# Kernel optimization log

Hardware: AMD Instinct MI355X
Metric: run time of the kernel (lower is better)

The kernel has to match this reference:

```python
import jax, jax.numpy as jnp
import numpy as np

N = 3072
FEAT = 128
E = 24576


def setup_inputs() -> dict:
    key = jax.random.key(0)
    k1, k2, k3, k4 = jax.random.split(key, 4)
    x = jax.random.normal(k1, (N, FEAT), dtype=jnp.float32)
    edge_index = jax.random.randint(k2, (2, E), 0, N, dtype=jnp.int32)
    batch = jnp.zeros((N,), dtype=jnp.int32)
    # lin: Linear(2*FEAT, 1)
    w = jax.random.normal(k3, (2 * FEAT,), dtype=jnp.float32) / np.sqrt(2 * FEAT)
    b = jax.random.normal(k4, (), dtype=jnp.float32) * 0.01
    return {"x": x, "edge_index": edge_index, "batch": batch, "w": w, "b": b}


def _cc_labels(adj):
    """Connected-component labels via min-label propagation + pointer jumping.
    Labels equal the minimum node index of each component, so ranking them by
    value reproduces scipy's first-occurrence component ordering."""
    n = adj.shape[0]
    adj = jax.lax.stop_gradient(adj)

    def body(state):
        labels, _ = state
        neigh = jnp.where(adj > 0, labels[None, :], n).min(axis=1)  # [n]
        new = jnp.minimum(labels, neigh)
        new = jnp.minimum(new, new[new])  # pointer jumping
        return new, jnp.any(new != labels)

    labels, _ = jax.lax.while_loop(lambda s: s[1], body,
                                   (jnp.arange(n), jnp.array(True)))
    return labels


def reference(x, edge_index, batch, w, b):
    n, f = x.shape
    idx = jnp.arange(n)
    src, dst = edge_index[0], edge_index[1]
    # undirected: duplicate each edge in both directions (coalesce in the
    # original dedups; dense scatter-set below is equivalent since duplicate
    # (u,v) edges get identical scores)
    s2 = jnp.concatenate([src, dst])
    d2 = jnp.concatenate([dst, src])
    # per-edge raw score: lin(concat(x[u], x[v]))  ->  tanh
    e = jnp.tanh(x[s2] @ w[:f] + x[d2] @ w[f:] + b)  # [2E]

    zero = jnp.zeros((n, n), dtype=x.dtype)
    A = zero.at[s2, d2].set(1.0).at[idx, idx].set(0.0)   # self-loops removed
    S = zero.at[s2, d2].set(e).at[idx, idx].set(0.0)
    contract = (e > 0.0).astype(x.dtype)                 # tanh -> threshold 0
    A_c = zero.at[s2, d2].max(contract).at[idx, idx].set(0.0)

    labels = _cc_labels(A_c)                             # min-node-index labels
    roots = (labels == idx).astype(jnp.int32)
    cluster = (jnp.cumsum(roots) - 1)[labels]            # consecutive 0..K-1
    C = jax.nn.one_hot(cluster, n, dtype=x.dtype)        # [n, n] (padded to n)

    single = (A_c.sum(axis=1) + A_c.sum(axis=0)) == 0    # isolated under contraction
    S = S.at[idx, idx].set(single.astype(x.dtype))

    X_new = (S @ C).T @ x                                # [n(padK), f]
    A_new = (C.T @ A @ C).at[idx, idx].set(0.0)          # dense coarsened adjacency
    new_batch = jnp.zeros((n,), dtype=batch.dtype).at[cluster].max(batch)
    return X_new, A_new, new_batch, cluster
```

## Files before the change

### kernel.cpp

```cpp
#include <hip/hip_runtime.h>
#include <math.h>

#define N 3072
#define FEAT 128
#define NE 24576
#define PSTRIDE 64
#define EPT 24
#define DOTB 768
#define OUTZ4 2458368
#define ZB3 608
#define GATB 192

__device__ __forceinline__ void wave_agg_add(bool valid, int key, float val,
                                             float* base, int stride, int off) {
    int lane = threadIdx.x & 63;
    unsigned long long active = __ballot(valid ? 1 : 0);
    while (active) {
        int leader = __ffsll(active) - 1;
        int lkey = __shfl(key, leader);
        bool mine = valid && (key == lkey);
        unsigned long long grp = __ballot(mine ? 1 : 0);
        float v = mine ? val : 0.0f;
        #pragma unroll
        for (int o = 32; o; o >>= 1) v += __shfl_xor(v, o);
        if (lane == leader)
            atomicAdd(&base[(size_t)lkey * stride + off], v);
        active &= ~grp;
    }
}

__global__ void k_init(const float* __restrict__ x, const float* __restrict__ w,
                       float* __restrict__ a, float* __restrict__ c,
                       float4* __restrict__ zws) {
    int b = blockIdx.x, t = threadIdx.x;
    if (b < DOTB) {
        int node = b * 4 + (t >> 6);
        int lane = t & 63;
        const float* xi = x + node * FEAT;
        float pa = xi[lane] * w[lane] + xi[lane + 64] * w[lane + 64];
        float pc = xi[lane] * w[FEAT + lane] + xi[lane + 64] * w[FEAT + lane + 64];
        for (int off = 32; off; off >>= 1) {
            pa += __shfl_down(pa, off);
            pc += __shfl_down(pc, off);
        }
        if (lane == 0) { a[node] = pa; c[node] = pc; }
    } else {
        float4 z = {0.f, 0.f, 0.f, 0.f};
        #pragma unroll
        for (int k = 0; k < 6; ++k) zws[k * 256 + t] = z;
    }
}

__global__ void k_edge_pairs(const int* __restrict__ ei, const float* __restrict__ a,
                             const float* __restrict__ c, const float* __restrict__ bb,
                             unsigned* __restrict__ ep, int* __restrict__ notsingle,
                             int* __restrict__ pcnt, unsigned long long* __restrict__ ptab) {
    int t = blockIdx.x * blockDim.x + threadIdx.x;
    if (t >= NE) return;
    int u = ei[t], v = ei[NE + t];
    unsigned wpk = (unsigned)u | ((unsigned)v << 12);
    if (u != v) {
        float b = bb[0];
        float su = a[u] + c[v] + b;
        float sv = a[v] + c[u] + b;
        unsigned fu = (su > 0.f) ? 1u : 0u;
        unsigned fv = (sv > 0.f) ? 1u : 0u;
        wpk |= (fu << 24) | (fv << 25);
        if (fu | fv) { notsingle[u] = 1; notsingle[v] = 1; }
        float eu = tanhf(su);
        int sl = atomicAdd(&pcnt[v], 1);
        if (sl < PSTRIDE)
            ptab[(size_t)v * PSTRIDE + sl] =
                ((unsigned long long)__float_as_uint(eu) << 32) | (unsigned)u;
        float ev2 = tanhf(sv);
        sl = atomicAdd(&pcnt[u], 1);
        if (sl < PSTRIDE)
            ptab[(size_t)u * PSTRIDE + sl] =
                ((unsigned long long)__float_as_uint(ev2) << 32) | (unsigned)v;
    }
    ep[t] = wpk;
}

__global__ void __launch_bounds__(1024)
k_prop_gather(const unsigned* __restrict__ ep, const float* __restrict__ x,
              const int* __restrict__ pcnt, const unsigned long long* __restrict__ ptab,
              const int* __restrict__ notsingle, float* __restrict__ y,
              unsigned long long* __restrict__ qmask, int* __restrict__ cluster,
              float* __restrict__ out_cluster, float4* __restrict__ zout) {
    __shared__ int lab[N];
    __shared__ int ssum[1024];
    __shared__ unsigned short rk[N];
    __shared__ int sh_p[16 * 64];
    __shared__ int flag;
    int t = threadIdx.x, blk = blockIdx.x;
    int wv = t >> 6, lane = t & 63;
    if (blk == 0) {
        unsigned er[EPT];
        unsigned act = 0;
        #pragma unroll
        for (int j = 0; j < EPT; ++j) {
            er[j] = ep[t + j * 1024];
            if (er[j] & 0x3000000u) act |= (1u << j);
        }
        for (int i = t; i < N; i += 1024) lab[i] = i;
        for (;;) {
            __syncthreads();
            if (t == 0) flag = 0;
            __syncthreads();
            unsigned rem = act;
            while (rem) {
                int j = __ffs(rem) - 1;
                rem &= rem - 1;
                unsigned wpk = er[j];
                int u = wpk & 0xFFF, v = (wpk >> 12) & 0xFFF;
                int lu = lab[u], lv = lab[v];
                if ((lu | lv) == 0) { act &= ~(1u << j); continue; }
                if ((wpk & (1u << 24)) && lv < lu) { atomicMin(&lab[u], lv); flag = 1; }
                if ((wpk & (1u << 25)) && lu < lv) { atomicMin(&lab[v], lu); flag = 1; }
            }
            for (int i = t; i < N; i += 1024) {
                int m = lab[i];
                if (m == 0) continue;
                int mm = lab[m];
                while (mm < m) { m = mm; mm = lab[m]; }
                if (m < lab[i]) { atomicMin(&lab[i], m); flag = 1; }
            }
            __syncthreads();
            if (!flag) break;
        }
        int i0 = 3 * t;
        int r0 = (lab[i0] == i0);
        int r1 = (lab[i0 + 1] == i0 + 1);
        int r2 = (lab[i0 + 2] == i0 + 2);
        int s = r0 + r1 + r2;
        ssum[t] = s;
        __syncthreads();
        for (int off = 1; off < 1024; off <<= 1) {
            int val = (t >= off) ? ssum[t - off] : 0;
            __syncthreads();
            ssum[t] += val;
            __syncthreads();
        }
        int run = ssum[t] - s;
        run += r0; rk[i0]     = (unsigned short)(run - 1);
        run += r1; rk[i0 + 1] = (unsigned short)(run - 1);
        run += r2; rk[i0 + 2] = (unsigned short)(run - 1);
        __syncthreads();
        for (int j = t; j < N; j += 1024) {
            int cl = rk[lab[j]];
            cluster[j] = cl;
            out_cluster[j] = (float)cl;
        }
    } else if (blk <= GATB) {
        int q = (blk - 1) * 16 + wv;
        int cnt = pcnt[q]; if (cnt > PSTRIDE) cnt = PSTRIDE;
        const unsigned long long* row = ptab + (size_t)q * PSTRIDE;
        int myp = -1 - lane;
        float mye = 0.f;
        if (lane < cnt) {
            unsigned long long s = row[lane];
            myp = (int)(s & 0xFFFFFFFFu);
            mye = __uint_as_float((unsigned)(s >> 32));
        }
        sh_p[wv * 64 + lane] = myp;
        bool dup = false;
        for (int j = 0; j < lane && !dup; ++j)
            dup = (sh_p[wv * 64 + j] == myp);
        bool valid = (lane < cnt) && !dup;
        unsigned long long m = __ballot(valid ? 1 : 0);
        if (lane == 0) qmask[q] = m;
        float acc0 = 0.f, acc1 = 0.f;
        for (int j = 0; j < cnt; ++j) {
            if (!((m >> j) & 1ull)) continue;
            int p = __shfl(myp, j);
            float e = __shfl(mye, j);
            const float* xp = x + p * FEAT;
            acc0 += e * xp[lane];
            acc1 += e * xp[lane + 64];
        }
        if (!notsingle[q]) {
            const float* xq = x + q * FEAT;
            acc0 += xq[lane];
            acc1 += xq[lane + 64];
        }
        float* yq = y + q * FEAT;
        yq[lane] = acc0;
        yq[lane + 64] = acc1;
    } else {
        float4 z = {0.f, 0.f, 0.f, 0.f};
        int base = (blk - GATB - 1) * 4096;
        #pragma unroll
        for (int k = 0; k < 4; ++k) {
            int idx = base + k * 1024 + t;
            if (idx < OUTZ4) zout[idx] = z;
        }
    }
}

__global__ void k_reduce_anew(const float* __restrict__ y, const int* __restrict__ cluster,
                              const int* __restrict__ pcnt,
                              const unsigned long long* __restrict__ ptab,
                              const unsigned long long* __restrict__ qmask,
                              float* __restrict__ Xnew, float* __restrict__ Anew) {
    int gid = blockIdx.x * blockDim.x + threadIdx.x;
    int wid = gid >> 6, lane = gid & 63;
    if (wid < 6144) {
        int f = wid & (FEAT - 1);
        int chunk = wid >> 7;
        int q = chunk * 64 + lane;
        wave_agg_add(true, cluster[q], y[q * FEAT + f], Xnew, FEAT, f);
    } else {
        int q = wid - 6144;
        int cnt = pcnt[q]; if (cnt > PSTRIDE) cnt = PSTRIDE;
        unsigned long long m = qmask[q];
        bool valid = (lane < cnt) && ((m >> lane) & 1ull);
        int p = 0;
        if (valid) p = (int)(ptab[(size_t)q * PSTRIDE + lane] & 0xFFFFFFFFu);
        int cq = cluster[q];
        int cp = valid ? cluster[p] : 0;
        valid = valid && (cp != cq);
        wave_agg_add(valid, cp * N + cq, 1.0f, Anew, 1, 0);
    }
}

extern "C" void kernel_launch(void* const* d_in, const int* in_sizes, int n_in,
                              void* d_out, int out_size, void* d_ws, size_t ws_size,
                              hipStream_t stream) {
    const float* x  = (const float*)d_in[0];
    const int*   ei = (const int*)d_in[1];
    const float* w  = (const float*)d_in[3];
    const float* bb = (const float*)d_in[4];

    char* ws = (char*)d_ws;
    size_t off = 0;
    int* pcnt     = (int*)(ws + off);      off += (size_t)N * 4;
    int* notsing  = (int*)(ws + off);      off += (size_t)N * 4;
    float* a      = (float*)(ws + off);    off += (size_t)N * 4;
    float* c      = (float*)(ws + off);    off += (size_t)N * 4;
    int* cluster  = (int*)(ws + off);      off += (size_t)N * 4;
    unsigned* ep  = (unsigned*)(ws + off); off += (size_t)NE * 4;
    unsigned long long* qmask = (unsigned long long*)(ws + off); off += (size_t)N * 8;
    float* y      = (float*)(ws + off);    off += (size_t)N * FEAT * 4;
    unsigned long long* ptab = (unsigned long long*)(ws + off); off += (size_t)N * PSTRIDE * 8;

    float* Xnew        = (float*)d_out;
    float* Anew        = Xnew + (size_t)N * FEAT;
    float* out_cluster = Anew + (size_t)N * N + N;

    k_init<<<DOTB + 1, 256, 0, stream>>>(x, w, a, c, (float4*)ws);
    k_edge_pairs<<<NE / 256, 256, 0, stream>>>(ei, a, c, bb, ep, notsing, pcnt, ptab);
    k_prop_gather<<<1 + GATB + ZB3, 1024, 0, stream>>>(ep, x, pcnt, ptab, notsing, y,
                                                       qmask, cluster, out_cluster,
                                                       (float4*)d_out);
    k_reduce_anew<<<(9216 * 64) / 1024, 1024, 0, stream>>>(y, cluster, pcnt, ptab,
                                                           qmask, Xnew, Anew);
}
```

Before: 146.2 us.

## Fuse four kernels into two using grid-level spin-wait flags

Merges the dot-product, edge-pair and output-zeroing kernels into one launch, where the edge blocks spin on an atomic counter until every dot block has finished. It also merges label propagation, neighbor gather and the Xnew/Anew atomic reduction into one launch, where all blocks wait on completion counters before the reduction phase. The edge-relaxation loop is unrolled into forward and reverse sweeps over register-held edges, which may cut the number of propagation rounds. The aim is to remove launch and inter-kernel gaps. In exchange the reduction now runs on far fewer waves, and the spin-waits assume all blocks are co-resident, which risks a hang if they are not.

Result: slower. 284.6 us (+94.6%).

```diff
diff --git a/kernel.cpp b/kernel.cpp
--- a/kernel.cpp
+++ b/kernel.cpp
@@ -5,11 +5,16 @@
 #define FEAT 128
 #define NE 24576
 #define PSTRIDE 64
-#define EPT 24
 #define DOTB 768
+#define EDGB 96
 #define OUTZ4 2458368
-#define ZB3 608
+#define OZB 2401
 #define GATB 192
+#define K2B (1 + GATB)
+#define RWAVES (K2B * 16)
+
+#define FOR24(M)  M(0)M(1)M(2)M(3)M(4)M(5)M(6)M(7)M(8)M(9)M(10)M(11)M(12)M(13)M(14)M(15)M(16)M(17)M(18)M(19)M(20)M(21)M(22)M(23)
+#define FOR24R(M) M(23)M(22)M(21)M(20)M(19)M(18)M(17)M(16)M(15)M(14)M(13)M(12)M(11)M(10)M(9)M(8)M(7)M(6)M(5)M(4)M(3)M(2)M(1)M(0)
 
 __device__ __forceinline__ void wave_agg_add(bool valid, int key, float val,
                                              float* base, int stride, int off) {
@@ -29,11 +34,21 @@
     }
 }
 
-__global__ void k_init(const float* __restrict__ x, const float* __restrict__ w,
-                       float* __restrict__ a, float* __restrict__ c,
-                       float4* __restrict__ zws) {
+__device__ __forceinline__ int ctrl_ld(const int* p) {
+    return __hip_atomic_load(p, __ATOMIC_RELAXED, __HIP_MEMORY_SCOPE_AGENT);
+}
+
+__global__ void k_initez(const float* __restrict__ x, const float* __restrict__ w,
+                         const int* __restrict__ ei, const float* __restrict__ bb,
+                         float* __restrict__ a, float* __restrict__ c,
+                         unsigned* __restrict__ ep, int* __restrict__ notsingle,
+                         int* __restrict__ pcnt, unsigned long long* __restrict__ ptab,
+                         float4* __restrict__ zout, float4* __restrict__ zws,
+                         int* __restrict__ ctrl) {
     int b = blockIdx.x, t = threadIdx.x;
     if (b < DOTB) {
+        float4 z = {0.f, 0.f, 0.f, 0.f};
+        if (b < 6) zws[b * 256 + t] = z;
         int node = b * 4 + (t >> 6);
         int lane = t & 63;
         const float* xi = x + node * FEAT;
@@ -44,49 +59,55 @@
             pc += __shfl_down(pc, off);
         }
         if (lane == 0) { a[node] = pa; c[node] = pc; }
+        __syncthreads();
+        __threadfence();
+        if (t == 0) atomicAdd(&ctrl[0], 1);
+    } else if (b < DOTB + EDGB) {
+        if (t == 0)
+            while (ctrl_ld(&ctrl[0]) < DOTB) __builtin_amdgcn_s_sleep(2);
+        __syncthreads();
+        __threadfence();
+        int s = (b - DOTB) * 256 + t;
+        int u = ei[s], v = ei[NE + s];
+        unsigned wpk = (unsigned)u | ((unsigned)v << 12);
+        if (u != v) {
+            float bias = bb[0];
+            float su = a[u] + c[v] + bias;
+            float sv = a[v] + c[u] + bias;
+            unsigned fu = (su > 0.f) ? 1u : 0u;
+            unsigned fv = (sv > 0.f) ? 1u : 0u;
+            wpk |= (fu << 24) | (fv << 25);
+            if (fu | fv) { notsingle[u] = 1; notsingle[v] = 1; }
+            float eu = tanhf(su);
+            int sl = atomicAdd(&pcnt[v], 1);
+            if (sl < PSTRIDE)
+                ptab[(size_t)v * PSTRIDE + sl] =
+                    ((unsigned long long)__float_as_uint(eu) << 32) | (unsigned)u;
+            float ev2 = tanhf(sv);
+            sl = atomicAdd(&pcnt[u], 1);
+            if (sl < PSTRIDE)
+                ptab[(size_t)u * PSTRIDE + sl] =
+                    ((unsigned long long)__float_as_uint(ev2) << 32) | (unsigned)v;
+        }
+        ep[s] = wpk;
     } else {
         float4 z = {0.f, 0.f, 0.f, 0.f};
+        int base = (b - DOTB - EDGB) * 1024;
         #pragma unroll
-        for (int k = 0; k < 6; ++k) zws[k * 256 + t] = z;
-    }
-}
-
-__global__ void k_edge_pairs(const int* __restrict__ ei, const float* __restrict__ a,
-                             const float* __restrict__ c, const float* __restrict__ bb,
-                             unsigned* __restrict__ ep, int* __restrict__ notsingle,
-                             int* __restrict__ pcnt, unsigned long long* __restrict__ ptab) {
-    int t = blockIdx.x * blockDim.x + threadIdx.x;
-    if (t >= NE) return;
-    int u = ei[t], v = ei[NE + t];
-    unsigned wpk = (unsigned)u | ((unsigned)v << 12);
-    if (u != v) {
-        float b = bb[0];
-        float su = a[u] + c[v] + b;
-        float sv = a[v] + c[u] + b;
-        unsigned fu = (su > 0.f) ? 1u : 0u;
-        unsigned fv = (sv > 0.f) ? 1u : 0u;
-        wpk |= (fu << 24) | (fv << 25);
-        if (fu | fv) { notsingle[u] = 1; notsingle[v] = 1; }
-        float eu = tanhf(su);
-        int sl = atomicAdd(&pcnt[v], 1);
-        if (sl < PSTRIDE)
-            ptab[(size_t)v * PSTRIDE + sl] =
-                ((unsigned long long)__float_as_uint(eu) << 32) | (unsigned)u;
-        float ev2 = tanhf(sv);
-        sl = atomicAdd(&pcnt[u], 1);
-        if (sl < PSTRIDE)
-            ptab[(size_t)u * PSTRIDE + sl] =
-                ((unsigned long long)__float_as_uint(ev2) << 32) | (unsigned)v;
-    }
-    ep[t] = wpk;
+        for (int k = 0; k < 4; ++k) {
+            int idx = base + k * 256 + t;
+            if (idx < OUTZ4) zout[idx] = z;
+        }
+    }
 }
 
 __global__ void __launch_bounds__(1024)
-k_prop_gather(const unsigned* __restrict__ ep, const float* __restrict__ x,
-              const int* __restrict__ pcnt, const unsigned long long* __restrict__ ptab,
-              const int* __restrict__ notsingle, float* __restrict__ y,
-              unsigned long long* __restrict__ qmask, int* __restrict__ cluster,
-              float* __restrict__ out_cluster, float4* __restrict__ zout) {
+k_pgr(const unsigned* __restrict__ ep, const float* __restrict__ x,
+      const int* __restrict__ pcnt, const unsigned long long* __restrict__ ptab,
+      const int* __restrict__ notsingle, float* __restrict__ y,
+      unsigned long long* __restrict__ qmask, int* __restrict__ cluster,
+      float* __restrict__ out_cluster, float* __restrict__ Xnew,
+      float* __restrict__ Anew, int* __restrict__ ctrl) {
     __shared__ int lab[N];
     __shared__ int ssum[1024];
     __shared__ unsigned short rk[N];
@@ -95,29 +116,26 @@
     int t = threadIdx.x, blk = blockIdx.x;
     int wv = t >> 6, lane = t & 63;
     if (blk == 0) {
-        unsigned er[EPT];
         unsigned act = 0;
-        #pragma unroll
-        for (int j = 0; j < EPT; ++j) {
-            er[j] = ep[t + j * 1024];
-            if (er[j] & 0x3000000u) act |= (1u << j);
-        }
+        #define LDE(j) unsigned e##j = ep[t + (j) * 1024]; \
+                       if (e##j & 0x3000000u) act |= (1u << (j));
+        FOR24(LDE)
         for (int i = t; i < N; i += 1024) lab[i] = i;
         for (;;) {
             __syncthreads();
             if (t == 0) flag = 0;
             __syncthreads();
-            unsigned rem = act;
-            while (rem) {
-                int j = __ffs(rem) - 1;
-                rem &= rem - 1;
-                unsigned wpk = er[j];
-                int u = wpk & 0xFFF, v = (wpk >> 12) & 0xFFF;
-                int lu = lab[u], lv = lab[v];
-                if ((lu | lv) == 0) { act &= ~(1u << j); continue; }
-                if ((wpk & (1u << 24)) && lv < lu) { atomicMin(&lab[u], lv); flag = 1; }
-                if ((wpk & (1u << 25)) && lu < lv) { atomicMin(&lab[v], lu); flag = 1; }
-            }
+            #define RLX(j) if (act & (1u << (j))) { \
+                int u_ = (int)(e##j & 0xFFFu); \
+                int v_ = (int)((e##j >> 12) & 0xFFFu); \
+                int lu_ = lab[u_], lv_ = lab[v_]; \
+                if ((lu_ | lv_) == 0) { act &= ~(1u << (j)); } \
+                else { \
+                    if ((e##j & (1u << 24)) && lv_ < lu_) { atomicMin(&lab[u_], lv_); flag = 1; } \
+                    if ((e##j & (1u << 25)) && lu_ < lv_) { atomicMin(&lab[v_], lu_); flag = 1; } \
+                } }
+            FOR24(RLX)
+            FOR24R(RLX)
             for (int i = t; i < N; i += 1024) {
                 int m = lab[i];
                 if (m == 0) continue;
@@ -151,7 +169,10 @@
             cluster[j] = cl;
             out_cluster[j] = (float)cl;
         }
-    } else if (blk <= GATB) {
+        __syncthreads();
+        __threadfence();
+        if (t == 0) atomicAdd(&ctrl[2], 1);
+    } else {
         int q = (blk - 1) * 16 + wv;
         int cnt = pcnt[q]; if (cnt > PSTRIDE) cnt = PSTRIDE;
         const unsigned long long* row = ptab + (size_t)q * PSTRIDE;
@@ -186,40 +207,34 @@
         float* yq = y + q * FEAT;
         yq[lane] = acc0;
         yq[lane + 64] = acc1;
-    } else {
-        float4 z = {0.f, 0.f, 0.f, 0.f};
-        int base = (blk - GATB - 1) * 4096;
-        #pragma unroll
-        for (int k = 0; k < 4; ++k) {
-            int idx = base + k * 1024 + t;
-            if (idx < OUTZ4) zout[idx] = z;
-        }
-    }
-}
-
-__global__ void k_reduce_anew(const float* __restrict__ y, const int* __restrict__ cluster,
-                              const int* __restrict__ pcnt,
-                              const unsigned long long* __restrict__ ptab,
-                              const unsigned long long* __restrict__ qmask,
-                              float* __restrict__ Xnew, float* __restrict__ Anew) {
-    int gid = blockIdx.x * blockDim.x + threadIdx.x;
-    int wid = gid >> 6, lane = gid & 63;
-    if (wid < 6144) {
-        int f = wid & (FEAT - 1);
-        int chunk = wid >> 7;
-        int q = chunk * 64 + lane;
-        wave_agg_add(true, cluster[q], y[q * FEAT + f], Xnew, FEAT, f);
-    } else {
-        int q = wid - 6144;
-        int cnt = pcnt[q]; if (cnt > PSTRIDE) cnt = PSTRIDE;
-        unsigned long long m = qmask[q];
-        bool valid = (lane < cnt) && ((m >> lane) & 1ull);
-        int p = 0;
-        if (valid) p = (int)(ptab[(size_t)q * PSTRIDE + lane] & 0xFFFFFFFFu);
-        int cq = cluster[q];
-        int cp = valid ? cluster[p] : 0;
-        valid = valid && (cp != cq);
-        wave_agg_add(valid, cp * N + cq, 1.0f, Anew, 1, 0);
+        __syncthreads();
+        __threadfence();
+        if (t == 0) atomicAdd(&ctrl[1], 1);
+    }
+    if (t == 0) {
+        while (ctrl_ld(&ctrl[1]) < GATB) __builtin_amdgcn_s_sleep(2);
+        while (ctrl_ld(&ctrl[2]) < 1)    __builtin_amdgcn_s_sleep(2);
+    }
+    __syncthreads();
+    __threadfence();
+    for (int gw = blk * 16 + wv; gw < 9216; gw += RWAVES) {
+        if (gw < 6144) {
+            int f = gw & (FEAT - 1);
+            int chunk = gw >> 7;
+            int q = chunk * 64 + lane;
+            wave_agg_add(true, cluster[q], y[q * FEAT + f], Xnew, FEAT, f);
+        } else {
+            int q = gw - 6144;
+            int cnt = pcnt[q]; if (cnt > PSTRIDE) cnt = PSTRIDE;
+            unsigned long long m = qmask[q];
+            bool valid = (lane < cnt) && ((m >> lane) & 1ull);
+            int p = 0;
+            if (valid) p = (int)(ptab[(size_t)q * PSTRIDE + lane] & 0xFFFFFFFFu);
+            int cq = cluster[q];
+            int cp = valid ? cluster[p] : 0;
+            valid = valid && (cp != cq);
+            wave_agg_add(valid, cp * N + cq, 1.0f, Anew, 1, 0);
+        }
     }
 }
 
@@ -233,6 +248,7 @@
 
     char* ws = (char*)d_ws;
     size_t off = 0;
+    int* ctrl     = (int*)(ws + off);      off += 16;
     int* pcnt     = (int*)(ws + off);      off += (size_t)N * 4;
     int* notsing  = (int*)(ws + off);      off += (size_t)N * 4;
     float* a      = (float*)(ws + off);    off += (size_t)N * 4;
@@ -247,11 +263,10 @@
     float* Anew        = Xnew + (size_t)N * FEAT;
     float* out_cluster = Anew + (size_t)N * N + N;
 
-    k_init<<<DOTB + 1, 256, 0, stream>>>(x, w, a, c, (float4*)ws);
-    k_edge_pairs<<<NE / 256, 256, 0, stream>>>(ei, a, c, bb, ep, notsing, pcnt, ptab);
-    k_prop_gather<<<1 + GATB + ZB3, 1024, 0, stream>>>(ep, x, pcnt, ptab, notsing, y,
-                                                       qmask, cluster, out_cluster,
-                                                       (float4*)d_out);
-    k_reduce_anew<<<(9216 * 64) / 1024, 1024, 0, stream>>>(y, cluster, pcnt, ptab,
-                                                           qmask, Xnew, Anew);
-}
+    hipMemsetAsync(ctrl, 0, 16, stream);
+    k_initez<<<DOTB + EDGB + OZB, 256, 0, stream>>>(x, w, ei, bb, a, c, ep, notsing,
+                                                    pcnt, ptab, (float4*)d_out,
+                                                    (float4*)pcnt, ctrl);
+    k_pgr<<<K2B, 1024, 0, stream>>>(ep, x, pcnt, ptab, notsing, y, qmask, cluster,
+                                    out_cluster, Xnew, Anew, ctrl);
+}
```

## Split connected-component labeling into giant-component BFS plus residual label propagation

Applied to the files above, without the earlier changes.

The single-block component labeling now first grows the component containing node 0 as a shared-memory bitmask, using directed reachability over the contracted edges. It then collects the leftover edges and nodes outside that component into compact shared lists and runs min-label propagation with pointer jumping only over them, falling back to a full edge sweep if the residual list overflows. The aim is to cut the per-iteration cost of label propagation, since the giant component is settled cheaply with bit operations. In exchange, edges are reloaded from global memory instead of held in registers, and shared memory use and code complexity both grow.

New measurement: 134.0 us. 1.09x faster.

```diff
diff --git a/kernel.cpp b/kernel.cpp
--- a/kernel.cpp
+++ b/kernel.cpp
@@ -5,11 +5,11 @@
 #define FEAT 128
 #define NE 24576
 #define PSTRIDE 64
-#define EPT 24
 #define DOTB 768
 #define OUTZ4 2458368
 #define ZB3 608
 #define GATB 192
+#define RESCAP 4096
 
 __device__ __forceinline__ void wave_agg_add(bool valid, int key, float val,
                                              float* base, int stride, int off) {
@@ -88,21 +88,19 @@
               unsigned long long* __restrict__ qmask, int* __restrict__ cluster,
               float* __restrict__ out_cluster, float4* __restrict__ zout) {
     __shared__ int lab[N];
+    __shared__ unsigned Vw[N / 32];
+    __shared__ unsigned res[RESCAP];
+    __shared__ unsigned short rnodes[N];
     __shared__ int ssum[1024];
     __shared__ unsigned short rk[N];
     __shared__ int sh_p[16 * 64];
-    __shared__ int flag;
+    __shared__ int flag, rescnt, rncnt;
     int t = threadIdx.x, blk = blockIdx.x;
     int wv = t >> 6, lane = t & 63;
     if (blk == 0) {
-        unsigned er[EPT];
-        unsigned act = 0;
-        #pragma unroll
-        for (int j = 0; j < EPT; ++j) {
-            er[j] = ep[t + j * 1024];
-            if (er[j] & 0x3000000u) act |= (1u << j);
-        }
-        for (int i = t; i < N; i += 1024) lab[i] = i;
+        if (t < N / 32) Vw[t] = (t == 0) ? 1u : 0u;
+        if (t == 0) { rescnt = 0; rncnt = 0; }
+        unsigned act = 0x00FFFFFFu;
         for (;;) {
             __syncthreads();
             if (t == 0) flag = 0;
@@ -111,19 +109,90 @@
             while (rem) {
                 int j = __ffs(rem) - 1;
                 rem &= rem - 1;
-                unsigned wpk = er[j];
+                unsigned wpk = ep[t + j * 1024];
+                if (!(wpk & 0x3000000u)) { act &= ~(1u << j); continue; }
                 int u = wpk & 0xFFF, v = (wpk >> 12) & 0xFFF;
-                int lu = lab[u], lv = lab[v];
-                if ((lu | lv) == 0) { act &= ~(1u << j); continue; }
-                if ((wpk & (1u << 24)) && lv < lu) { atomicMin(&lab[u], lv); flag = 1; }
-                if ((wpk & (1u << 25)) && lu < lv) { atomicMin(&lab[v], lu); flag = 1; }
-            }
-            for (int i = t; i < N; i += 1024) {
-                int m = lab[i];
-                if (m == 0) continue;
-                int mm = lab[m];
-                while (mm < m) { m = mm; mm = lab[m]; }
-                if (m < lab[i]) { atomicMin(&lab[i], m); flag = 1; }
+                unsigned pu = (Vw[u >> 5] >> (u & 31)) & 1u;
+                unsigned pv = (Vw[v >> 5] >> (v & 31)) & 1u;
+                if ((wpk & (1u << 24)) && pv && !pu) {
+                    atomicOr(&Vw[u >> 5], 1u << (u & 31)); pu = 1; flag = 1;
+                }
+                if ((wpk & (1u << 25)) && pu && !pv) {
+                    atomicOr(&Vw[v >> 5], 1u << (v & 31)); pv = 1; flag = 1;
+                }
+                bool done = (pu || !(wpk & (1u << 24))) && (pv || !(wpk & (1u << 25)));
+                if (done) act &= ~(1u << j);
+            }
+            __syncthreads();
+            if (!flag) break;
+        }
+        unsigned rem = act;
+        while (rem) {
+            int j = __ffs(rem) - 1;
+            rem &= rem - 1;
+            unsigned wpk = ep[t + j * 1024];
+            int u = wpk & 0xFFF, v = (wpk >> 12) & 0xFFF;
+            unsigned pu = (Vw[u >> 5] >> (u & 31)) & 1u;
+            unsigned pv = (Vw[v >> 5] >> (v & 31)) & 1u;
+            if ((wpk & (1u << 24)) && !pu) {
+                int pos = atomicAdd(&rescnt, 1);
+                if (pos < RESCAP) res[pos] = (unsigned)u | ((unsigned)v << 12);
+            }
+            if ((wpk & (1u << 25)) && !pv) {
+                int pos = atomicAdd(&rescnt, 1);
+                if (pos < RESCAP) res[pos] = (unsigned)v | ((unsigned)u << 12);
+            }
+        }
+        for (int i = t; i < N; i += 1024) {
+            unsigned inV = (Vw[i >> 5] >> (i & 31)) & 1u;
+            lab[i] = inV ? 0 : i;
+            if (!inV) {
+                int pos = atomicAdd(&rncnt, 1);
+                rnodes[pos] = (unsigned short)i;
+            }
+        }
+        __syncthreads();
+        int nres = rescnt < RESCAP ? rescnt : RESCAP;
+        bool ovf = (rescnt > RESCAP);
+        int nrn = rncnt;
+        for (;;) {
+            __syncthreads();
+            if (t == 0) flag = 0;
+            __syncthreads();
+            if (!ovf) {
+                for (int k = t; k < nres; k += 1024) {
+                    unsigned w2 = res[k];
+                    int p = w2 & 0xFFF, q = (w2 >> 12) & 0xFFF;
+                    int lq = lab[q];
+                    if (lq < lab[p]) { atomicMin(&lab[p], lq); flag = 1; }
+                }
+                for (int k = t; k < nrn; k += 1024) {
+                    int i = rnodes[k];
+                    int m = lab[i];
+                    int mm = lab[m];
+                    while (mm < m) { m = mm; mm = lab[m]; }
+                    if (m < lab[i]) { atomicMin(&lab[i], m); flag = 1; }
+                }
+            } else {
+                for (int j = 0; j < 24; ++j) {
+                    unsigned wpk = ep[t + j * 1024];
+                    int u = wpk & 0xFFF, v = (wpk >> 12) & 0xFFF;
+                    if (wpk & (1u << 24)) {
+                        int lv = lab[v];
+                        if (lv < lab[u]) { atomicMin(&lab[u], lv); flag = 1; }
+                    }
+                    if (wpk & (1u << 25)) {
+                        int lu = lab[u];
+                        if (lu < lab[v]) { atomicMin(&lab[v], lu); flag = 1; }
+                    }
+                }
+                for (int i = t; i < N; i += 1024) {
+                    int m = lab[i];
+                    if (m == 0) continue;
+                    int mm = lab[m];
+                    while (mm < m) { m = mm; mm = lab[m]; }
+                    if (m < lab[i]) { atomicMin(&lab[i], m); flag = 1; }
+                }
             }
             __syncthreads();
             if (!flag) break;
@@ -247,7 +316,7 @@
     float* Anew        = Xnew + (size_t)N * FEAT;
     float* out_cluster = Anew + (size_t)N * N + N;
 
-    k_init<<<DOTB + 1, 256, 0, stream>>>(x, w, a, c, (float4*)ws);
+    k_init<<<DOTB + 1, 256, 0, stream>>>(x, w, a, c, (float4*)pcnt);
     k_edge_pairs<<<NE / 256, 256, 0, stream>>>(ei, a, c, bb, ep, notsing, pcnt, ptab);
     k_prop_gather<<<1 + GATB + ZB3, 1024, 0, stream>>>(ep, x, pcnt, ptab, notsing, y,
                                                        qmask, cluster, out_cluster,
```
